# Kernel optimization log

Measured on AMD Instinct MI355X. Metric: run time of the kernel, lower is better.

The kernel has to match this reference:

```python
import jax, jax.numpy as jnp
import numpy as np

N_NODES = 100000
N_EDGES = 800000
IN_DIM = 128
HID = 16
HEADS1 = 8
HEADS2 = 10
OUT_DIM = 10
NEG_SLOPE = 0.2  # PyG GATConv default


def segment_softmax(logits, seg, num_segments):
    # logits: [E, H], seg: [E] destination node ids
    m = jax.ops.segment_max(logits, seg, num_segments=num_segments)  # [N, H]
    m = jnp.where(jnp.isfinite(m), m, 0.0)
    e = jnp.exp(logits - m[seg])
    s = jax.ops.segment_sum(e, seg, num_segments=num_segments)  # [N, H]
    return e / (s[seg] + 1e-16)


def gat_conv(x, src, dst, W, a_src, a_dst, bias, heads, out_ch, concat):
    N = x.shape[0]
    h = (x @ W).reshape(N, heads, out_ch)  # [N, H, C]
    alpha_src = jnp.einsum('nhc,hc->nh', h, a_src)
    alpha_dst = jnp.einsum('nhc,hc->nh', h, a_dst)
    logits = jax.nn.leaky_relu(alpha_src[src] + alpha_dst[dst], NEG_SLOPE)  # [E, H]
    alpha = segment_softmax(logits, dst, N)  # [E, H]
    msg = h[src] * alpha[:, :, None]  # [E, H, C]
    out = jax.ops.segment_sum(msg, dst, num_segments=N)  # [N, H, C]
    out = out.reshape(N, heads * out_ch) if concat else out.mean(axis=1)
    return out + bias


def setup_inputs() -> dict:
    key = jax.random.key(0)
    ks = jax.random.split(key, 12)
    g = 0.1
    return {
        'x': jax.random.normal(ks[0], (N_NODES, IN_DIM), jnp.float32),
        'edge_index': jax.random.randint(ks[1], (2, N_EDGES), 0, N_NODES, jnp.int64),
        'labels': jax.random.randint(ks[2], (N_NODES,), 0, OUT_DIM, jnp.int64),
        'train_mask': jax.random.randint(ks[3], (N_NODES,), 0, 2, jnp.int32).astype(bool),
        'W1': jax.random.normal(ks[4], (IN_DIM, HEADS1 * HID), jnp.float32) * g,
        'a_src1': jax.random.normal(ks[5], (HEADS1, HID), jnp.float32) * g,
        'a_dst1': jax.random.normal(ks[6], (HEADS1, HID), jnp.float32) * g,
        'b1': jnp.zeros((HEADS1 * HID,), jnp.float32),
        'W2': jax.random.normal(ks[7], (HEADS1 * HID, HEADS2 * OUT_DIM), jnp.float32) * g,
        'a_src2': jax.random.normal(ks[8], (HEADS2, OUT_DIM), jnp.float32) * g,
        'a_dst2': jax.random.normal(ks[9], (HEADS2, OUT_DIM), jnp.float32) * g,
        'b2': jnp.zeros((OUT_DIM,), jnp.float32),
    }


def reference(x, edge_index, labels, train_mask, W1, a_src1, a_dst1, b1, W2, a_src2, a_dst2, b2):
    # dropout layers are identity in eval mode
    src, dst = edge_index[0], edge_index[1]
    emb1 = gat_conv(x, src, dst, W1, a_src1, a_dst1, b1, HEADS1, HID, concat=True)   # [N, H1*HID]
    h = jax.nn.elu(emb1)
    emb2 = gat_conv(h, src, dst, W2, a_src2, a_dst2, b2, HEADS2, OUT_DIM, concat=False)  # [N, OUT]
    logp = jax.nn.log_softmax(emb2, axis=-1)
    ce = -jnp.take_along_axis(logp, labels[:, None], axis=-1)[:, 0]  # [N]
    m = train_mask.astype(emb2.dtype)
    loss = jnp.sum(ce * m) / jnp.sum(m)
    return (loss, emb1, emb2)
```

## Files before the change

### kernel.cpp

```cpp
#include <hip/hip_runtime.h>
#include <hip/hip_bf16.h>
#include <math.h>

#define N_NODES 100000
#define N_EDGES 800000
#define NB_SCAN ((N_NODES + 1023) / 1024)
#define GB1 ((N_NODES + 31)/32)
#define SB  ((N_EDGES + 255)/256)
#define PG1 1024

typedef __bf16 bf16x8 __attribute__((ext_vector_type(8)));
typedef float  f32x4  __attribute__((ext_vector_type(4)));

__device__ __forceinline__ float lrelu(float v){ return v > 0.f ? v : 0.2f*v; }
__device__ __forceinline__ float eluf(float v){ return v > 0.f ? v : (__expf(v) - 1.f); }

__device__ __forceinline__ unsigned short f2bf(float f){
    union { float f; unsigned u; } v; v.f = f;
    unsigned r = (v.u + 0x7fff + ((v.u >> 16) & 1)) >> 16;
    return (unsigned short)r;
}
__device__ __forceinline__ float bf2f(unsigned short u){
    union { unsigned u; float f; } v; v.u = ((unsigned)u) << 16;
    return v.f;
}
__device__ __forceinline__ unsigned char f2fp8(float v){
    return (unsigned char)(__builtin_amdgcn_cvt_pk_fp8_f32(v, v, 0, false) & 0xff);
}

__global__ __launch_bounds__(256) void setup_kernel(
    const float* __restrict__ W1, const float* __restrict__ W2,
    unsigned short* __restrict__ wt1, unsigned short* __restrict__ wt2,
    int* __restrict__ counts, float* __restrict__ lacc)
{
    int i = blockIdx.x*256 + threadIdx.x;
    if (i < N_NODES) counts[i] = 0;
    if (i < 4) lacc[i] = 0.f;
    if (i < 128*128){
        int n = i >> 7, k = i & 127;
        wt1[i] = f2bf(W1[k*128 + n]);
    }
    if (i < 112*128){
        int n = i >> 7, k = i & 127;
        wt2[i] = (n < 100) ? f2bf(W2[k*100 + n]) : (unsigned short)0;
    }
}

__global__ __launch_bounds__(256) void count_kernel(const int* __restrict__ ei,
                                                    int* __restrict__ counts,
                                                    int* __restrict__ rank){
    int e = blockIdx.x*256 + threadIdx.x;
    if (e < N_EDGES){
        int d = ei[N_EDGES + e];
        rank[e] = atomicAdd(&counts[d], 1);
    }
}

__global__ __launch_bounds__(1024) void scan_blocks_kernel(const int* __restrict__ counts,
                                                           int* __restrict__ exoffs,
                                                           int* __restrict__ bsums){
    __shared__ int buf[1024];
    int t = threadIdx.x;
    int gid = blockIdx.x*1024 + t;
    int v = (gid < N_NODES) ? counts[gid] : 0;
    buf[t] = v;
    __syncthreads();
    #pragma unroll
    for (int off = 1; off < 1024; off <<= 1){
        int u = (t >= off) ? buf[t-off] : 0;
        __syncthreads();
        buf[t] += u;
        __syncthreads();
    }
    if (gid < N_NODES) exoffs[gid] = buf[t] - v;
    if (t == 1023) bsums[blockIdx.x] = buf[1023];
}

__global__ void scan_sums_kernel(const int* __restrict__ bsums, int* __restrict__ bpre){
    if (threadIdx.x == 0){
        int run = 0;
        #pragma unroll 4
        for (int b = 0; b < NB_SCAN; b++){ int v = bsums[b]; bpre[b] = run; run += v; }
    }
}

__global__ __launch_bounds__(1024) void scan_add_kernel(const int* __restrict__ exoffs,
                                                        const int* __restrict__ bpre,
                                                        int* __restrict__ offs){
    int gid = blockIdx.x*1024 + threadIdx.x;
    if (gid < N_NODES){
        offs[gid] = exoffs[gid] + bpre[blockIdx.x];
    }
    if (gid == 0) offs[N_NODES] = N_EDGES;
}

__global__ __launch_bounds__(256) void scatter_kernel(
    const int* __restrict__ ei, const int* __restrict__ offs, const int* __restrict__ rank,
    int* __restrict__ csr_src)
{
    int e = blockIdx.x*256 + threadIdx.x;
    if (e >= N_EDGES) return;
    int s = ei[e];
    int d = ei[N_EDGES + e];
    csr_src[offs[d] + rank[e]] = s;
}

__global__ __launch_bounds__(256) void gemm1_mfma(
    const float* __restrict__ x, const unsigned short* __restrict__ wt1,
    const float* __restrict__ a_src, const float* __restrict__ a_dst,
    unsigned short* __restrict__ h1bf, float* __restrict__ as1, float* __restrict__ ad1)
{
    __shared__ unsigned short Al[32*128];
    __shared__ unsigned short Bl[128*128];
    int t = threadIdx.x;

    #pragma unroll
    for (int i = 0; i < 8; i++){
        int idx = (i*256 + t)*8;
        int n = idx >> 7, c = idx & 127;
        bf16x8 v = *(const bf16x8*)(wt1 + n*128 + c);
        int byte = (n*256 + c*2) ^ ((n&7)<<4);
        *(bf16x8*)((char*)Bl + byte) = v;
    }

    int wv = t >> 6, l = t & 63;
    int wm = wv >> 1, wn = wv & 1;
    int lr = l & 15, lg = l >> 4;

    for (int tile = blockIdx.x; tile < GB1; tile += PG1){
        int row0 = tile*32;
        #pragma unroll
        for (int i = 0; i < 2; i++){
            int idx = (i*256 + t)*8;
            int r = idx >> 7, c = idx & 127;
            int grow = row0 + r;
            bf16x8 v;
            if (grow < N_NODES){
                const float4* p = (const float4*)(x + (size_t)grow*128 + c);
                float4 f0 = p[0], f1 = p[1];
                v[0]=(__bf16)f0.x; v[1]=(__bf16)f0.y; v[2]=(__bf16)f0.z; v[3]=(__bf16)f0.w;
                v[4]=(__bf16)f1.x; v[5]=(__bf16)f1.y; v[6]=(__bf16)f1.z; v[7]=(__bf16)f1.w;
            } else {
                #pragma unroll
                for (int j = 0; j < 8; j++) v[j] = (__bf16)0.f;
            }
            int byte = (r*256 + c*2) ^ ((r&7)<<4);
            *(bf16x8*)((char*)Al + byte) = v;
        }
        __syncthreads();

        bf16x8 af[4];
        #pragma unroll
        for (int ks = 0; ks < 4; ks++){
            int r = wm*16 + lr;
            int byte = (r*256 + (ks*32 + lg*8)*2) ^ ((r&7)<<4);
            af[ks] = *(const bf16x8*)((const char*)Al + byte);
        }
        f32x4 acc[4];
        #pragma unroll
        for (int nt = 0; nt < 4; nt++){
            acc[nt] = (f32x4){0.f,0.f,0.f,0.f};
            #pragma unroll
            for (int ks = 0; ks < 4; ks++){
                int n = wn*64 + nt*16 + lr;
                int byte = (n*256 + (ks*32 + lg*8)*2) ^ ((n&7)<<4);
                bf16x8 bfv = *(const bf16x8*)((const char*)Bl + byte);
                acc[nt] = __builtin_amdgcn_mfma_f32_16x16x32_bf16(af[ks], bfv, acc[nt], 0, 0, 0);
            }
        }
        int orow_base = row0 + wm*16 + lg*4;
        #pragma unroll
        for (int nt = 0; nt < 4; nt++){
            int colb = wn*64 + nt*16;
            int head = colb >> 4;
            float avs = a_src[colb + lr];
            float avd = a_dst[colb + lr];
            #pragma unroll
            for (int r = 0; r < 4; r++){
                int grow = orow_base + r;
                float v = acc[nt][r];
                if (grow < N_NODES) h1bf[(size_t)grow*128 + colb + lr] = f2bf(v);
                float ps = v*avs, pd = v*avd;
                ps += __shfl_xor(ps,1); ps += __shfl_xor(ps,2); ps += __shfl_xor(ps,4); ps += __shfl_xor(ps,8);
                pd += __shfl_xor(pd,1); pd += __shfl_xor(pd,2); pd += __shfl_xor(pd,4); pd += __shfl_xor(pd,8);
                if (lr == 0 && grow < N_NODES){
                    as1[grow*8 + head] = ps;
                    ad1[grow*8 + head] = pd;
                }
            }
        }
        __syncthreads();
    }
}

__global__ __launch_bounds__(256) void agg1_kernel(
    const int* __restrict__ offs, const int* __restrict__ csr_src,
    const float* __restrict__ as1, const float* __restrict__ ad1,
    const unsigned short* __restrict__ h1bf, const float* __restrict__ b1,
    float* __restrict__ emb1_out )
{
    int wave = threadIdx.x >> 6;
    int lane = threadIdx.x & 63;
    int d = blockIdx.x*4 + wave;
    if (d >= N_NODES) return;
    int h = lane >> 3;
    int col = 2*lane;
    int e0 = offs[d], e1 = offs[d+1];
    float ad = ad1[d*8 + h];
    float acc0 = 0.f, acc1 = 0.f, wsum = 0.f;

    for (int base = e0; base < e1; base += 64){
        int ii = base + lane;
        int sv = (ii < e1) ? csr_src[ii] : 0;
        int n = min(64, e1 - base);
        int i = 0;
        for (; i + 3 < n; i += 4){
            int s0 = __shfl(sv, i);
            int s1 = __shfl(sv, i+1);
            int s2 = __shfl(sv, i+2);
            int s3 = __shfl(sv, i+3);
            float l0 = as1[s0*8 + h];
            float l1 = as1[s1*8 + h];
            float l2 = as1[s2*8 + h];
            float l3 = as1[s3*8 + h];
            unsigned hv0 = *(const unsigned*)(h1bf + (size_t)s0*128 + col);
            unsigned hv1 = *(const unsigned*)(h1bf + (size_t)s1*128 + col);
            unsigned hv2 = *(const unsigned*)(h1bf + (size_t)s2*128 + col);
            unsigned hv3 = *(const unsigned*)(h1bf + (size_t)s3*128 + col);
            float w0 = __expf(lrelu(l0 + ad));
            float w1 = __expf(lrelu(l1 + ad));
            float w2 = __expf(lrelu(l2 + ad));
            float w3 = __expf(lrelu(l3 + ad));
            acc0 += w0*bf2f((unsigned short)hv0) + w1*bf2f((unsigned short)hv1)
                  + w2*bf2f((unsigned short)hv2) + w3*bf2f((unsigned short)hv3);
            acc1 += w0*bf2f((unsigned short)(hv0>>16)) + w1*bf2f((unsigned short)(hv1>>16))
                  + w2*bf2f((unsigned short)(hv2>>16)) + w3*bf2f((unsigned short)(hv3>>16));
            wsum += (w0 + w1) + (w2 + w3);
        }
        for (; i < n; i++){
            int s0 = __shfl(sv, i);
            float w0 = __expf(lrelu(as1[s0*8 + h] + ad));
            unsigned hv0 = *(const unsigned*)(h1bf + (size_t)s0*128 + col);
            acc0 += w0*bf2f((unsigned short)hv0);
            acc1 += w0*bf2f((unsigned short)(hv0>>16));
            wsum += w0;
        }
    }
    float inv = 1.f/(wsum + 1e-16f);
    emb1_out[(size_t)d*128 + col]     = acc0*inv + b1[col];
    emb1_out[(size_t)d*128 + col + 1] = acc1*inv + b1[col+1];
}

__global__ __launch_bounds__(256) void gemm2_mfma(
    const float* __restrict__ emb1g , const unsigned short* __restrict__ wt2,
    const float* __restrict__ a_src2, const float* __restrict__ a_dst2,
    unsigned char* __restrict__ h2f8, float* __restrict__ as2, float* __restrict__ ad2)
{
    __shared__ __align__(16) char smem[36864];
    unsigned short* Al = (unsigned short*)smem;
    unsigned short* Bl = Al + 32*128;
    float* Hl = (float*)smem;

    int t = threadIdx.x;
    int row0 = blockIdx.x*32;

    #pragma unroll
    for (int i = 0; i < 2; i++){
        int idx = (i*256 + t)*8;
        int r = idx >> 7, c = idx & 127;
        int grow = row0 + r;
        bf16x8 v;
        if (grow < N_NODES){
            const float4* p = (const float4*)(emb1g + (size_t)grow*128 + c);
            float4 f0 = p[0], f1 = p[1];
            v[0]=(__bf16)eluf(f0.x); v[1]=(__bf16)eluf(f0.y); v[2]=(__bf16)eluf(f0.z); v[3]=(__bf16)eluf(f0.w);
            v[4]=(__bf16)eluf(f1.x); v[5]=(__bf16)eluf(f1.y); v[6]=(__bf16)eluf(f1.z); v[7]=(__bf16)eluf(f1.w);
        } else {
            #pragma unroll
            for (int j = 0; j < 8; j++) v[j] = (__bf16)0.f;
        }
        int byte = (r*256 + c*2) ^ ((r&7)<<4);
        *(bf16x8*)((char*)Al + byte) = v;
    }
    #pragma unroll
    for (int i = 0; i < 7; i++){
        int idx = (i*256 + t)*8;
        int n = idx >> 7, c = idx & 127;
        bf16x8 v = *(const bf16x8*)(wt2 + n*128 + c);
        int byte = (n*256 + c*2) ^ ((n&7)<<4);
        *(bf16x8*)((char*)Bl + byte) = v;
    }
    __syncthreads();

    int wv = t >> 6, l = t & 63;
    int wm = wv >> 1, wn = wv & 1;
    int lr = l & 15, lg = l >> 4;
    bf16x8 af[4];
    #pragma unroll
    for (int ks = 0; ks < 4; ks++){
        int r = wm*16 + lr;
        int byte = (r*256 + (ks*32 + lg*8)*2) ^ ((r&7)<<4);
        af[ks] = *(const bf16x8*)((const char*)Al + byte);
    }
    int ntmax = wn ? 3 : 4;
    f32x4 acc[4];
    for (int nt = 0; nt < ntmax; nt++){
        acc[nt] = (f32x4){0.f,0.f,0.f,0.f};
        #pragma unroll
        for (int ks = 0; ks < 4; ks++){
            int n = wn*64 + nt*16 + lr;
            int byte = (n*256 + (ks*32 + lg*8)*2) ^ ((n&7)<<4);
            bf16x8 bfv = *(const bf16x8*)((const char*)Bl + byte);
            acc[nt] = __builtin_amdgcn_mfma_f32_16x16x32_bf16(af[ks], bfv, acc[nt], 0, 0, 0);
        }
    }
    int orow_base = row0 + wm*16 + lg*4;
    for (int nt = 0; nt < ntmax; nt++){
        int col = wn*64 + nt*16 + lr;
        if (col < 100){
            #pragma unroll
            for (int r = 0; r < 4; r++){
                int grow = orow_base + r;
                if (grow < N_NODES) h2f8[(size_t)grow*100 + col] = f2fp8(acc[nt][r]);
            }
        }
    }
    __syncthreads();
    for (int nt = 0; nt < ntmax; nt++){
        int col = wn*64 + nt*16 + lr;
        int rbase = wm*16 + lg*4;
        #pragma unroll
        for (int r = 0; r < 4; r++) Hl[(rbase + r)*113 + col] = acc[nt][r];
    }
    __syncthreads();
    for (int task = t; task < 320; task += 256){
        int row = task/10, h = task - row*10;
        int grow = row0 + row;
        if (grow < N_NODES){
            const float* p = &Hl[row*113 + h*10];
            float s = 0.f, dd = 0.f;
            #pragma unroll
            for (int c = 0; c < 10; c++){
                float v = p[c];
                s  += v*a_src2[h*10 + c];
                dd += v*a_dst2[h*10 + c];
            }
            as2[grow*10 + h] = s;
            ad2[grow*10 + h] = dd;
        }
    }
}

__global__ __launch_bounds__(256) void agg2_kernel(
    const int* __restrict__ offs, const int* __restrict__ csr_src,
    const float* __restrict__ as2, const float* __restrict__ ad2,
    const unsigned char* __restrict__ h2f8, const float* __restrict__ b2,
    float* __restrict__ emb2_out)
{
    __shared__ float sval[4][100];
    int wv = threadIdx.x >> 6;
    int lane = threadIdx.x & 63;
    int d = blockIdx.x*4 + wv;
    if (d >= N_NODES) return;
    int c0 = 2*lane;
    bool act = lane < 50;
    int h = lane/5; if (h > 9) h = 9;
    float adh = act ? ad2[d*10 + h] : 0.f;
    int e0 = offs[d], e1 = offs[d+1];
    float acc0 = 0.f, acc1 = 0.f, wsum = 0.f;

    for (int base = e0; base < e1; base += 64){
        int ii = base + lane;
        int sv = (ii < e1) ? csr_src[ii] : 0;
        int n = min(64, e1 - base);
        int i = 0;
        for (; i + 3 < n; i += 4){
            int s0 = __shfl(sv, i);
            int s1 = __shfl(sv, i+1);
            int s2 = __shfl(sv, i+2);
            int s3 = __shfl(sv, i+3);
            float l0=0.f,l1=0.f,l2=0.f,l3=0.f;
            int v0=0,v1=0,v2=0,v3=0;
            if (act){
                l0 = as2[s0*10 + h]; l1 = as2[s1*10 + h];
                l2 = as2[s2*10 + h]; l3 = as2[s3*10 + h];
                v0 = *(const unsigned short*)(h2f8 + (size_t)s0*100 + c0);
                v1 = *(const unsigned short*)(h2f8 + (size_t)s1*100 + c0);
                v2 = *(const unsigned short*)(h2f8 + (size_t)s2*100 + c0);
                v3 = *(const unsigned short*)(h2f8 + (size_t)s3*100 + c0);
            }
            float w0 = __expf(lrelu(l0 + adh));
            float w1 = __expf(lrelu(l1 + adh));
            float w2 = __expf(lrelu(l2 + adh));
            float w3 = __expf(lrelu(l3 + adh));
            acc0 += w0*__builtin_amdgcn_cvt_f32_fp8(v0, 0) + w1*__builtin_amdgcn_cvt_f32_fp8(v1, 0)
                  + w2*__builtin_amdgcn_cvt_f32_fp8(v2, 0) + w3*__builtin_amdgcn_cvt_f32_fp8(v3, 0);
            acc1 += w0*__builtin_amdgcn_cvt_f32_fp8(v0, 1) + w1*__builtin_amdgcn_cvt_f32_fp8(v1, 1)
                  + w2*__builtin_amdgcn_cvt_f32_fp8(v2, 1) + w3*__builtin_amdgcn_cvt_f32_fp8(v3, 1);
            wsum += (w0 + w1) + (w2 + w3);
        }
        for (; i < n; i++){
            int s0 = __shfl(sv, i);
            float l0 = 0.f; int v0 = 0;
            if (act){
                l0 = as2[s0*10 + h];
                v0 = *(const unsigned short*)(h2f8 + (size_t)s0*100 + c0);
            }
            float w0 = __expf(lrelu(l0 + adh));
            acc0 += w0*__builtin_amdgcn_cvt_f32_fp8(v0, 0);
            acc1 += w0*__builtin_amdgcn_cvt_f32_fp8(v0, 1);
            wsum += w0;
        }
    }
    if (act){
        float inv = 1.f/(wsum + 1e-16f);
        sval[wv][c0]   = acc0*inv;
        sval[wv][c0+1] = acc1*inv;
    }
    __syncthreads();
    if (lane < 10){
        float s = 0.f;
        #pragma unroll
        for (int hh = 0; hh < 10; hh++) s += sval[wv][hh*10 + lane];
        emb2_out[(size_t)d*10 + lane] = s*0.1f + b2[lane];
    }
}

__global__ __launch_bounds__(256) void loss_kernel(
    const float* __restrict__ emb2, const int* __restrict__ labels,
    const int* __restrict__ mask, float* __restrict__ acc)
{
    int i = blockIdx.x*256 + threadIdx.x;
    float num = 0.f, den = 0.f;
    if (i < N_NODES && mask[i] != 0){
        const float* v = emb2 + (size_t)i*10;
        float m = v[0];
        #pragma unroll
        for (int c = 1; c < 10; c++) m = fmaxf(m, v[c]);
        float s = 0.f;
        #pragma unroll
        for (int c = 0; c < 10; c++) s += __expf(v[c]-m);
        float lse = m + __logf(s);
        num = lse - v[labels[i]];
        den = 1.f;
    }
    #pragma unroll
    for (int o = 32; o >= 1; o >>= 1){ num += __shfl_down(num, o); den += __shfl_down(den, o); }
    if ((threadIdx.x & 63) == 0){
        atomicAdd(&acc[0], num);
        atomicAdd(&acc[1], den);
    }
}

__global__ void finalize_kernel(const float* __restrict__ acc, float* __restrict__ out0){
    out0[0] = acc[0]/acc[1];
}

extern "C" void kernel_launch(void* const* d_in, const int* in_sizes, int n_in,
                              void* d_out, int out_size, void* d_ws, size_t ws_size,
                              hipStream_t stream) {
    const float* x      = (const float*)d_in[0];
    const int*   ei     = (const int*)d_in[1];
    const int*   labels = (const int*)d_in[2];
    const int*   mask   = (const int*)d_in[3];
    const float* W1     = (const float*)d_in[4];
    const float* a_src1 = (const float*)d_in[5];
    const float* a_dst1 = (const float*)d_in[6];
    const float* b1     = (const float*)d_in[7];
    const float* W2     = (const float*)d_in[8];
    const float* a_src2 = (const float*)d_in[9];
    const float* a_dst2 = (const float*)d_in[10];
    const float* b2     = (const float*)d_in[11];

    float* out  = (float*)d_out;
    float* emb1 = out + 1;
    float* emb2 = out + 1 + (size_t)N_NODES*128;

    unsigned short* h1bf = (unsigned short*)d_ws;
    unsigned char*  h2f8 = (unsigned char*)(h1bf + (size_t)N_NODES*128);
    float* as1  = (float*)(h2f8 + (size_t)N_NODES*100);
    float* ad1  = as1 + (size_t)N_NODES*8;
    float* as2  = ad1 + (size_t)N_NODES*8;
    float* ad2  = as2 + (size_t)N_NODES*10;
    float* lacc = ad2 + (size_t)N_NODES*10;
    int* counts = (int*)(lacc + 4);
    int* offs   = counts + N_NODES;
    int* rank   = offs + N_NODES + 1;
    int* csr    = rank + N_EDGES;
    int* exoffs = csr + N_EDGES;
    int* bsums  = exoffs + N_NODES;
    int* bpre   = bsums + NB_SCAN;
    unsigned short* wt1 = (unsigned short*)(bpre + NB_SCAN);
    unsigned short* wt2 = wt1 + 128*128;

    setup_kernel<<<(N_NODES+255)/256, 256, 0, stream>>>(W1, W2, wt1, wt2, counts, lacc);
    count_kernel<<<SB, 256, 0, stream>>>(ei, counts, rank);
    scan_blocks_kernel<<<NB_SCAN, 1024, 0, stream>>>(counts, exoffs, bsums);
    scan_sums_kernel<<<1, 64, 0, stream>>>(bsums, bpre);
    scan_add_kernel<<<NB_SCAN, 1024, 0, stream>>>(exoffs, bpre, offs);
    scatter_kernel<<<SB, 256, 0, stream>>>(ei, offs, rank, csr);

    gemm1_mfma<<<PG1, 256, 0, stream>>>(x, wt1, a_src1, a_dst1, h1bf, as1, ad1);
    agg1_kernel<<<(N_NODES + 3)/4, 256, 0, stream>>>(offs, csr, as1, ad1, h1bf, b1, emb1);
    gemm2_mfma<<<GB1, 256, 0, stream>>>(emb1, wt2, a_src2, a_dst2, h2f8, as2, ad2);
    agg2_kernel<<<(N_NODES + 3)/4, 256, 0, stream>>>(offs, csr, as2, ad2, h2f8, b2, emb2);
    loss_kernel<<<(N_NODES+255)/256, 256, 0, stream>>>(emb2, labels, mask, lacc);
    finalize_kernel<<<1, 1, 0, stream>>>(lacc, out);
}
```

Baseline: 267.0 us.

## Fuse loss into agg2, merge block-sum scan into scan_add, bin loss atomics

```diff
diff --git a/kernel.cpp b/kernel.cpp
--- a/kernel.cpp
+++ b/kernel.cpp
@@ -8,6 +8,7 @@
 #define GB1 ((N_NODES + 31)/32)
 #define SB  ((N_EDGES + 255)/256)
 #define PG1 1024
+#define NBINS 256
 
 typedef __bf16 bf16x8 __attribute__((ext_vector_type(8)));
 typedef float  f32x4  __attribute__((ext_vector_type(4)));
@@ -35,7 +36,7 @@
 {
     int i = blockIdx.x*256 + threadIdx.x;
     if (i < N_NODES) counts[i] = 0;
-    if (i < 4) lacc[i] = 0.f;
+    if (i < 2*NBINS) lacc[i] = 0.f;
     if (i < 128*128){
         int n = i >> 7, k = i & 127;
         wt1[i] = f2bf(W1[k*128 + n]);
@@ -76,20 +77,25 @@
     if (t == 1023) bsums[blockIdx.x] = buf[1023];
 }
 
-__global__ void scan_sums_kernel(const int* __restrict__ bsums, int* __restrict__ bpre){
-    if (threadIdx.x == 0){
-        int run = 0;
-        #pragma unroll 4
-        for (int b = 0; b < NB_SCAN; b++){ int v = bsums[b]; bpre[b] = run; run += v; }
-    }
-}
-
 __global__ __launch_bounds__(1024) void scan_add_kernel(const int* __restrict__ exoffs,
-                                                        const int* __restrict__ bpre,
+                                                        const int* __restrict__ bsums,
                                                         int* __restrict__ offs){
-    int gid = blockIdx.x*1024 + threadIdx.x;
+    __shared__ int sb[128];
+    int t = threadIdx.x;
+    if (t < 128){
+        int lim = min((int)blockIdx.x, NB_SCAN);
+        sb[t] = (t < lim) ? bsums[t] : 0;
+    }
+    __syncthreads();
+    #pragma unroll
+    for (int off = 64; off >= 1; off >>= 1){
+        if (t < off) sb[t] += sb[t + off];
+        __syncthreads();
+    }
+    int pre = sb[0];
+    int gid = blockIdx.x*1024 + t;
     if (gid < N_NODES){
-        offs[gid] = exoffs[gid] + bpre[blockIdx.x];
+        offs[gid] = exoffs[gid] + pre;
     }
     if (gid == 0) offs[N_NODES] = N_EDGES;
 }
@@ -355,13 +361,14 @@
     const int* __restrict__ offs, const int* __restrict__ csr_src,
     const float* __restrict__ as2, const float* __restrict__ ad2,
     const unsigned char* __restrict__ h2f8, const float* __restrict__ b2,
-    float* __restrict__ emb2_out)
+    const int* __restrict__ labels, const int* __restrict__ mask,
+    float* __restrict__ emb2_out, float* __restrict__ lacc)
 {
     __shared__ float sval[4][100];
+    __shared__ float bln[4], bld[4];
     int wv = threadIdx.x >> 6;
     int lane = threadIdx.x & 63;
     int d = blockIdx.x*4 + wv;
-    if (d >= N_NODES) return;
     int c0 = 2*lane;
     bool act = lane < 50;
     int h = lane/5; if (h > 9) h = 9;
@@ -422,38 +429,50 @@
         float s = 0.f;
         #pragma unroll
         for (int hh = 0; hh < 10; hh++) s += sval[wv][hh*10 + lane];
-        emb2_out[(size_t)d*10 + lane] = s*0.1f + b2[lane];
-    }
-}
-
-__global__ __launch_bounds__(256) void loss_kernel(
-    const float* __restrict__ emb2, const int* __restrict__ labels,
-    const int* __restrict__ mask, float* __restrict__ acc)
-{
-    int i = blockIdx.x*256 + threadIdx.x;
-    float num = 0.f, den = 0.f;
-    if (i < N_NODES && mask[i] != 0){
-        const float* v = emb2 + (size_t)i*10;
-        float m = v[0];
-        #pragma unroll
-        for (int c = 1; c < 10; c++) m = fmaxf(m, v[c]);
-        float s = 0.f;
-        #pragma unroll
-        for (int c = 0; c < 10; c++) s += __expf(v[c]-m);
-        float lse = m + __logf(s);
-        num = lse - v[labels[i]];
-        den = 1.f;
-    }
-    #pragma unroll
-    for (int o = 32; o >= 1; o >>= 1){ num += __shfl_down(num, o); den += __shfl_down(den, o); }
-    if ((threadIdx.x & 63) == 0){
-        atomicAdd(&acc[0], num);
-        atomicAdd(&acc[1], den);
-    }
-}
-
-__global__ void finalize_kernel(const float* __restrict__ acc, float* __restrict__ out0){
-    out0[0] = acc[0]/acc[1];
+        float val = s*0.1f + b2[lane];
+        emb2_out[(size_t)d*10 + lane] = val;
+        sval[wv][lane] = val;
+    }
+    __syncthreads();
+    if (lane == 0){
+        float num = 0.f, den = 0.f;
+        if (mask[d] != 0){
+            float m = sval[wv][0];
+            #pragma unroll
+            for (int c = 1; c < 10; c++) m = fmaxf(m, sval[wv][c]);
+            float ssum = 0.f;
+            #pragma unroll
+            for (int c = 0; c < 10; c++) ssum += __expf(sval[wv][c] - m);
+            num = (m + __logf(ssum)) - sval[wv][labels[d]];
+            den = 1.f;
+        }
+        bln[wv] = num; bld[wv] = den;
+    }
+    __syncthreads();
+    if (threadIdx.x == 0){
+        float n = bln[0]+bln[1]+bln[2]+bln[3];
+        float dd = bld[0]+bld[1]+bld[2]+bld[3];
+        if (dd != 0.f){
+            int bin = (blockIdx.x & (NBINS-1))*2;
+            atomicAdd(&lacc[bin], n);
+            atomicAdd(&lacc[bin+1], dd);
+        }
+    }
+}
+
+__global__ void finalize_kernel(const float* __restrict__ lacc, float* __restrict__ out0){
+    __shared__ float sn[4], sd[4];
+    int t = threadIdx.x;
+    float n = lacc[2*t], d = lacc[2*t+1];
+    #pragma unroll
+    for (int o = 32; o >= 1; o >>= 1){ n += __shfl_down(n, o); d += __shfl_down(d, o); }
+    if ((t & 63) == 0){ sn[t>>6] = n; sd[t>>6] = d; }
+    __syncthreads();
+    if (t == 0){
+        float N2 = sn[0]+sn[1]+sn[2]+sn[3];
+        float D2 = sd[0]+sd[1]+sd[2]+sd[3];
+        out0[0] = N2/D2;
+    }
 }
 
 extern "C" void kernel_launch(void* const* d_in, const int* in_sizes, int n_in,
@@ -483,27 +502,24 @@
     float* as2  = ad1 + (size_t)N_NODES*8;
     float* ad2  = as2 + (size_t)N_NODES*10;
     float* lacc = ad2 + (size_t)N_NODES*10;
-    int* counts = (int*)(lacc + 4);
+    int* counts = (int*)(lacc + 2*NBINS);
     int* offs   = counts + N_NODES;
     int* rank   = offs + N_NODES + 1;
     int* csr    = rank + N_EDGES;
     int* exoffs = csr + N_EDGES;
     int* bsums  = exoffs + N_NODES;
-    int* bpre   = bsums + NB_SCAN;
-    unsigned short* wt1 = (unsigned short*)(bpre + NB_SCAN);
+    unsigned short* wt1 = (unsigned short*)(bsums + NB_SCAN);
     unsigned short* wt2 = wt1 + 128*128;
 
     setup_kernel<<<(N_NODES+255)/256, 256, 0, stream>>>(W1, W2, wt1, wt2, counts, lacc);
     count_kernel<<<SB, 256, 0, stream>>>(ei, counts, rank);
     scan_blocks_kernel<<<NB_SCAN, 1024, 0, stream>>>(counts, exoffs, bsums);
-    scan_sums_kernel<<<1, 64, 0, stream>>>(bsums, bpre);
-    scan_add_kernel<<<NB_SCAN, 1024, 0, stream>>>(exoffs, bpre, offs);
+    scan_add_kernel<<<NB_SCAN, 1024, 0, stream>>>(exoffs, bsums, offs);
     scatter_kernel<<<SB, 256, 0, stream>>>(ei, offs, rank, csr);
 
     gemm1_mfma<<<PG1, 256, 0, stream>>>(x, wt1, a_src1, a_dst1, h1bf, as1, ad1);
     agg1_kernel<<<(N_NODES + 3)/4, 256, 0, stream>>>(offs, csr, as1, ad1, h1bf, b1, emb1);
     gemm2_mfma<<<GB1, 256, 0, stream>>>(emb1, wt2, a_src2, a_dst2, h2f8, as2, ad2);
-    agg2_kernel<<<(N_NODES + 3)/4, 256, 0, stream>>>(offs, csr, as2, ad2, h2f8, b2, emb2);
-    loss_kernel<<<(N_NODES+255)/256, 256, 0, stream>>>(emb2, labels, mask, lacc);
-    finalize_kernel<<<1, 1, 0, stream>>>(lacc, out);
-}
+    agg2_kernel<<<N_NODES/4, 256, 0, stream>>>(offs, csr, as2, ad2, h2f8, b2, labels, mask, emb2, lacc);
+    finalize_kernel<<<1, 256, 0, stream>>>(lacc, out);
+}
```

Result: faster. 234.9 us, median of 2 (-12.0%).
